# Kernel tuning notes

Measured on AMD Instinct MI355X. Metric: run time of the kernel, lower is better.

## Reference

```python
import jax, jax.numpy as jnp
import numpy as np
import math

B, T, D = 8, 2048, 1024
H, DH = 16, 64
DI = H * DH
EPS = 1e-6
LN_EPS = 1e-5


def setup_inputs() -> dict:
    key = jax.random.key(0)
    ks = jax.random.split(key, 8)
    def xavier(k, shape):
        fan_in, fan_out = shape[0], shape[1]
        bound = math.sqrt(6.0 / (fan_in + fan_out))
        return jax.random.uniform(k, shape, jnp.float32, -bound, bound)
    x = jax.random.normal(ks[0], (B, T, D), jnp.float32)
    Wq = xavier(ks[1], (D, DI))
    Wk = xavier(ks[2], (D, DI))
    Wv = xavier(ks[3], (D, DI))
    Wa = jax.random.normal(ks[4], (D, DI), jnp.float32) * 0.02
    ba = jnp.full((DI,), 3.0, jnp.float32)
    Wb = jax.random.normal(ks[5], (D, H), jnp.float32) * 0.02
    bb = jnp.zeros((H,), jnp.float32)
    raw_gamma_m = jnp.full((H,), math.log(0.99 / 0.01), jnp.float32)
    Wo = xavier(ks[6], (DI, D))
    ln_g = jnp.ones((D,), jnp.float32)
    ln_b = jnp.zeros((D,), jnp.float32)
    return {"x": x, "ln_g": ln_g, "ln_b": ln_b, "Wq": Wq, "Wk": Wk, "Wv": Wv,
            "Wa": Wa, "ba": ba, "Wb": Wb, "bb": bb,
            "raw_gamma_m": raw_gamma_m, "Wo": Wo}


def _layernorm(x, g, b):
    mu = jnp.mean(x, axis=-1, keepdims=True)
    var = jnp.mean(jnp.square(x - mu), axis=-1, keepdims=True)
    return (x - mu) * jax.lax.rsqrt(var + LN_EPS) * g + b


def _sokda_scan(q, k, v, alpha, beta, gamma_m):
    # q,k,v,alpha: (B,H,T,d); beta: (B,H,T); gamma_m: (H,)
    d = q.shape[-1]
    S0 = jnp.zeros((B, H, d, d), q.dtype)
    M0 = EPS * jnp.broadcast_to(jnp.eye(d, dtype=q.dtype), (B, H, d, d))
    gm = gamma_m[None, :, None, None]  # (1,H,1,1)

    def step(carry, xs):
        S, M = carry
        k_t, v_t, q_t, a_t, b_t = xs  # (B,H,d)x4, (B,H)
        kn = k_t / jnp.maximum(jnp.linalg.norm(k_t, axis=-1, keepdims=True), 1e-12)
        M = gm * M + kn[..., :, None] * kn[..., None, :]
        Mk = jnp.einsum('bhij,bhj->bhi', M, kn)
        k_tilde = Mk / jnp.maximum(jnp.linalg.norm(Mk, axis=-1, keepdims=True), EPS)
        S = a_t[..., None] * S  # diag(alpha) scaling of rows
        kproj = jnp.einsum('bhd,bhde->bhe', kn, S)  # k^T S
        bexp = b_t[..., None, None]
        S = S - bexp * k_tilde[..., :, None] * kproj[..., None, :]
        S = S + bexp * kn[..., :, None] * v_t[..., None, :]
        o = jnp.einsum('bhji,bhj->bhi', S, q_t)  # S^T q
        return (S, M), o

    # move time to leading axis for scan
    xs = (jnp.moveaxis(k, 2, 0), jnp.moveaxis(v, 2, 0), jnp.moveaxis(q, 2, 0),
          jnp.moveaxis(alpha, 2, 0), jnp.moveaxis(beta, 2, 0))
    _, outs = jax.lax.scan(step, (S0, M0), xs)  # outs: (T,B,H,d)
    return jnp.moveaxis(outs, 0, 2)  # (B,H,T,d)


def reference(x, ln_g, ln_b, Wq, Wk, Wv, Wa, ba, Wb, bb, raw_gamma_m, Wo):
    residual = x
    xn = _layernorm(x, ln_g, ln_b)
    def heads(y):
        return jnp.transpose(y.reshape(B, T, H, DH), (0, 2, 1, 3))  # (B,H,T,d)
    q = heads(xn @ Wq)
    k = heads(xn @ Wk)
    v = heads(xn @ Wv)
    alpha = jax.nn.sigmoid(heads(xn @ Wa + ba))
    beta = jnp.transpose(jax.nn.sigmoid(xn @ Wb + bb), (0, 2, 1))  # (B,H,T)
    gamma_m = jax.nn.sigmoid(raw_gamma_m)
    out = _sokda_scan(q, k, v, alpha, beta, gamma_m)  # (B,H,T,d)
    out = jnp.transpose(out, (0, 2, 1, 3)).reshape(B, T, DI)
    out = out @ Wo  # dropout is identity in eval mode
    return out + residual
```

## Files before the change

kernel.cpp:

```cpp
#include <hip/hip_runtime.h>

typedef unsigned short u16;
typedef unsigned int   u32;
typedef _Float16       f16;
typedef __attribute__((ext_vector_type(4))) _Float16 v4h;
typedef __attribute__((ext_vector_type(8))) _Float16 v8h;
typedef __attribute__((ext_vector_type(4))) float    v4f;

#define TT 2048
#define BB 8

static __device__ __forceinline__ float sigmoidf_(float x){
    return 1.0f / (1.0f + __expf(-x));
}
static __device__ __forceinline__ float allreduce64(float v){
    #pragma unroll
    for (int off = 32; off > 0; off >>= 1) v += __shfl_xor(v, off, 64);
    return v;
}

static __device__ __forceinline__ float wave_sum64(float x){
    int t;
    t = __builtin_amdgcn_update_dpp(0, __float_as_int(x), 0x111, 0xf, 0xf, true); x += __int_as_float(t);
    t = __builtin_amdgcn_update_dpp(0, __float_as_int(x), 0x112, 0xf, 0xf, true); x += __int_as_float(t);
    t = __builtin_amdgcn_update_dpp(0, __float_as_int(x), 0x114, 0xf, 0xf, true); x += __int_as_float(t);
    t = __builtin_amdgcn_update_dpp(0, __float_as_int(x), 0x118, 0xf, 0xf, true); x += __int_as_float(t);
    t = __builtin_amdgcn_update_dpp(0, __float_as_int(x), 0x142, 0xf, 0xf, true); x += __int_as_float(t);
    t = __builtin_amdgcn_update_dpp(0, __float_as_int(x), 0x143, 0xf, 0xf, true); x += __int_as_float(t);
    return __int_as_float(__builtin_amdgcn_readlane(__float_as_int(x), 63));
}
static __device__ __forceinline__ float rlane(float v, int lane){
    return __int_as_float(__builtin_amdgcn_readlane(__float_as_int(v), lane));
}

__global__ __launch_bounds__(256) void sentinel_fill(float* __restrict__ out, int n){
    int i = blockIdx.x * 256 + threadIdx.x;
    if (i < n) out[i] = 12345.0f;
}

__global__ __launch_bounds__(256) void ln_kernel(
    const float* __restrict__ x, const float* __restrict__ g,
    const float* __restrict__ bta, f16* __restrict__ xn)
{
    const int row = blockIdx.x;
    const int tid = threadIdx.x;
    const float4 v = ((const float4*)(x + (size_t)row * 1024))[tid];
    float s  = v.x + v.y + v.z + v.w;
    float s2 = v.x*v.x + v.y*v.y + v.z*v.z + v.w*v.w;
    #pragma unroll
    for (int off = 32; off > 0; off >>= 1){
        s  += __shfl_xor(s,  off, 64);
        s2 += __shfl_xor(s2, off, 64);
    }
    __shared__ float rs[4], rq[4];
    const int wv = tid >> 6, lane = tid & 63;
    if (lane == 0){ rs[wv] = s; rq[wv] = s2; }
    __syncthreads();
    s  = rs[0] + rs[1] + rs[2] + rs[3];
    s2 = rq[0] + rq[1] + rq[2] + rq[3];
    const float mu   = s * (1.0f / 1024.0f);
    const float var  = s2 * (1.0f / 1024.0f) - mu * mu;
    const float rstd = rsqrtf(var + 1e-5f);
    const float4 gv = ((const float4*)g)[tid];
    const float4 bv = ((const float4*)bta)[tid];
    v4h o;
    o.x = (f16)((v.x - mu) * rstd * gv.x + bv.x);
    o.y = (f16)((v.y - mu) * rstd * gv.y + bv.y);
    o.z = (f16)((v.z - mu) * rstd * gv.z + bv.z);
    o.w = (f16)((v.w - mu) * rstd * gv.w + bv.w);
    ((v4h*)(xn + (size_t)row * 1024))[tid] = o;
}

__global__ __launch_bounds__(256) void transpose5(
    const float* __restrict__ Wq, const float* __restrict__ Wk,
    const float* __restrict__ Wv, const float* __restrict__ Wa,
    const float* __restrict__ Wo, f16* __restrict__ wcat, f16* __restrict__ wot)
{
    __shared__ float tile[32][33];
    const int z = blockIdx.z;
    const float* src = (z==0)?Wq:(z==1)?Wk:(z==2)?Wv:(z==3)?Wa:Wo;
    f16* dst = (z < 4) ? (wcat + (size_t)z * 1024 * 1024) : wot;
    const int bx = blockIdx.x * 32, by = blockIdx.y * 32;
    const int tx = threadIdx.x, ty = threadIdx.y;
    #pragma unroll
    for (int i = 0; i < 4; ++i)
        tile[ty + i*8][tx] = src[(size_t)(by + ty + i*8) * 1024 + bx + tx];
    __syncthreads();
    #pragma unroll
    for (int i = 0; i < 4; ++i)
        dst[(size_t)(bx + ty + i*8) * 1024 + by + tx] = (f16)tile[tx][ty + i*8];
}

template<int MODE>
__global__ __launch_bounds__(256) void gemm_bt(
    const f16* __restrict__ A, const f16* __restrict__ Bt,
    int M, int N, int K,
    const float* __restrict__ ba, const float* __restrict__ resid,
    float* __restrict__ Cf,
    f16* __restrict__ Qb, f16* __restrict__ Kb,
    f16* __restrict__ Vb, f16* __restrict__ Ab)
{
    __shared__ f16 As[128 * 72];
    __shared__ f16 Bs[128 * 72];
    const int tid = threadIdx.x;
    const int bm = blockIdx.x, bn = blockIdx.y;
    const int wv = tid >> 6, lane = tid & 63;
    const int l15 = lane & 15, quad = lane >> 4;
    const int mb = (wv >> 1) * 64, nb = (wv & 1) * 64;
    v4f acc[4][4];
    const v4f vzero = {0.0f, 0.0f, 0.0f, 0.0f};
    #pragma unroll
    for (int i = 0; i < 4; ++i)
        #pragma unroll
        for (int j = 0; j < 4; ++j) acc[i][j] = vzero;

    const f16* Ag = A  + (size_t)bm * 128 * K;
    const f16* Bg = Bt + (size_t)bn * 128 * K;

    for (int k0 = 0; k0 < K; k0 += 64){
        __syncthreads();
        #pragma unroll
        for (int it = 0; it < 4; ++it){
            const int ch = tid + it * 256;
            const int r = ch >> 3, c = ch & 7;
            const uint4 da = *(const uint4*)(Ag + (size_t)r * K + k0 + c * 8);
            *(uint4*)(&As[r * 72 + c * 8]) = da;
            const uint4 db = *(const uint4*)(Bg + (size_t)r * K + k0 + c * 8);
            *(uint4*)(&Bs[r * 72 + c * 8]) = db;
        }
        __syncthreads();
        #pragma unroll
        for (int kk = 0; kk < 2; ++kk){
            v8h af[4], bfr[4];
            #pragma unroll
            for (int i = 0; i < 4; ++i){
                af[i]  = *(const v8h*)(&As[(mb + i*16 + l15) * 72 + kk*32 + quad*8]);
                bfr[i] = *(const v8h*)(&Bs[(nb + i*16 + l15) * 72 + kk*32 + quad*8]);
            }
            #pragma unroll
            for (int i = 0; i < 4; ++i)
                #pragma unroll
                for (int j = 0; j < 4; ++j)
                    acc[i][j] = __builtin_amdgcn_mfma_f32_16x16x32_f16(af[i], bfr[j], acc[i][j], 0, 0, 0);
        }
    }
    const int seg = (bn * 128) >> 10;
    f16* dst = (seg == 0) ? Qb : (seg == 1) ? Kb : (seg == 2) ? Vb : Ab;
    #pragma unroll
    for (int i = 0; i < 4; ++i){
        #pragma unroll
        for (int j = 0; j < 4; ++j){
            const int col = bn * 128 + nb + j * 16 + l15;
            const int c   = col & 1023;
            #pragma unroll
            for (int r = 0; r < 4; ++r){
                const int row = bm * 128 + mb + i * 16 + quad * 4 + r;
                float val = acc[i][j][r];
                if (MODE == 0){
                    if (seg == 3) val = sigmoidf_(val + ba[c]);
                    dst[(size_t)row * 1024 + c] = (f16)val;
                } else {
                    Cf[(size_t)row * N + col] = val + resid[(size_t)row * N + col];
                }
            }
        }
    }
}

__global__ __launch_bounds__(256) void beta_kernel(
    const f16* __restrict__ xn, const float* __restrict__ Wb,
    const float* __restrict__ bb, float* __restrict__ betaw)
{
    const int row = blockIdx.x;
    const int b = row >> 11, t = row & 2047;
    const int wv = threadIdx.x >> 6, lane = threadIdx.x & 63;
    const f16* xr = xn + (size_t)row * 1024;
    #pragma unroll
    for (int hh = 0; hh < 4; ++hh){
        const int h = wv * 4 + hh;
        float acc = 0.0f;
        #pragma unroll 4
        for (int k = lane; k < 1024; k += 64)
            acc += (float)xr[k] * Wb[k * 16 + h];
        acc = allreduce64(acc);
        if (lane == 0)
            betaw[((size_t)(b * 16 + h)) * 2048 + t] = sigmoidf_(acc + bb[h]);
    }
}

#define SC 16
__global__ __launch_bounds__(512, 2) void scan_kernel(
    const f16* __restrict__ Qb, const f16* __restrict__ Kb,
    const f16* __restrict__ Vb, const f16* __restrict__ Ab,
    const float* __restrict__ beta, const float* __restrict__ rgm,
    f16* __restrict__ O)
{
    const int chain = blockIdx.x;
    const int b = chain >> 4, h = chain & 15;
    const int tid = threadIdx.x;
    const int wid = __builtin_amdgcn_readfirstlane(tid) >> 6;
    const int l = tid & 63;
    const int jbase = wid << 3;
    const float gm = sigmoidf_(rgm[h]);
    const int l15 = l & 15, q4 = l >> 4;

    __shared__ f16 tQ[1024], tK[1024], tV[1024], tA[1024];
    __shared__ float betaT[SC], rnkT[SC];
    __shared__ float ktlT[1024];
    __shared__ float Gc[1024];
    __shared__ float mkP[8192];
    __shared__ f16 PhT[16*72], PlT[16*72], QhT[16*72], QlT[16*72];
    __shared__ f16 Wcat[16*136], Ucat[16*136];
    __shared__ f16 WTcat[64*40], UTcat[64*40];
    __shared__ f16 HTcat[64*40];
    __shared__ f16 VT[64*24];
    __shared__ f16 ZTcat[64*136];
    __shared__ f16 Cmcat[3*16*40];
    __shared__ float ZsT[64*68];
    __shared__ float Hs[16*68], Ob[16*68];
    __shared__ float C2s[16*17];

    float m[8];
    #pragma unroll
    for (int dd = 0; dd < 8; ++dd)
        m[dd] = (jbase + dd == l) ? 1e-6f : 0.0f;

    const size_t cbase = ((size_t)(b * TT)) * 1024 + h * 64;
    const int tens = tid >> 7, rem = tid & 127;
    const int str = rem >> 3, j4 = rem & 7;
    const f16* sg = (tens == 0) ? Qb : (tens == 1) ? Kb : (tens == 2) ? Vb : Ab;
    f16* sl = (tens == 0) ? tQ : (tens == 1) ? tK : (tens == 2) ? tV : tA;

    {
        const uint4 d0 = *(const uint4*)(sg + cbase + (size_t)str * 1024 + j4 * 8);
        *(uint4*)(sl + str * 64 + j4 * 8) = d0;
        if (tid < SC) betaT[tid] = beta[(size_t)chain * TT + tid];
        for (int i = tid; i < 64*68; i += 512) ZsT[i] = 0.0f;
        for (int i = tid; i < 64*136; i += 512) ZTcat[i] = (f16)0.0f;
    }

    #pragma unroll 1
    for (int t0 = 0; t0 < TT; t0 += SC){
        __syncthreads();

        #pragma unroll
        for (int rr = 0; rr < 2; ++rr){
            const int t = (wid << 1) + rr;
            const float kv = (float)tK[t * 64 + l];
            const float nk = wave_sum64(kv * kv);
            if (l == 0) rnkT[t] = __builtin_amdgcn_rcpf(fmaxf(sqrtf(nk), 1e-12f));
        }
        if (wid == 7){
            float g = 1.0f;
            #pragma unroll
            for (int t = 0; t < SC; ++t){
                g *= (float)tA[t * 64 + l];
                Gc[t * 64 + l] = g;
            }
        }
        __syncthreads();

        #pragma unroll
        for (int t = 0; t < SC; ++t){
            const float knl = (float)tK[t * 64 + l] * rnkT[t];
            float knj2[8];
            #pragma unroll
            for (int dd = 0; dd < 8; ++dd) knj2[dd] = rlane(knl, jbase + dd);
            float mk0 = 0.f, mk1 = 0.f;
            #pragma unroll
            for (int dd = 0; dd < 8; dd += 2){
                m[dd]     = fmaf(gm, m[dd],     knl * knj2[dd]);
                mk0 = fmaf(m[dd], knj2[dd], mk0);
                m[dd + 1] = fmaf(gm, m[dd + 1], knl * knj2[dd + 1]);
                mk1 = fmaf(m[dd + 1], knj2[dd + 1], mk1);
            }
            mkP[(t << 9) + (wid << 6) + l] = mk0 + mk1;
        }
        __syncthreads();

        #pragma unroll
        for (int rr = 0; rr < 2; ++rr){
            const int t = (wid << 1) + rr;
            float mkf = 0.f;
            #pragma unroll
            for (int w2 = 0; w2 < 8; ++w2) mkf += mkP[(t << 9) + (w2 << 6) + l];
            const float nmk = wave_sum64(mkf * mkf);
            ktlT[t * 64 + l] = mkf * __builtin_amdgcn_rcpf(fmaxf(sqrtf(nmk), 1e-6f));
        }
        #pragma unroll
        for (int half = 0; half < 2; ++half){
            const int idx = tid + half * 512;
            const int e = idx & 63, i = idx >> 6;
            VT[e * 24 + i] = tV[i * 64 + e];
        }
        __syncthreads();

        #pragma unroll
        for (int half = 0; half < 2; ++half){
            const int idx = tid + half * 512;
            const int t = idx >> 6, d = idx & 63;
            const float g    = Gc[t * 64 + d];
            const float invg = 1.0f / g;
            const float kn   = (float)tK[t * 64 + d] * rnkT[t];
            const float bt   = betaT[t];
            const float pv = kn * g;
            const float uv = bt * ktlT[t * 64 + d] * invg;
            const float wv = bt * kn * invg;
            const float qv = (float)tQ[t * 64 + d] * g;
            const f16 ph = (f16)pv, qh = (f16)qv, wh = (f16)wv, uh = (f16)uv;
            const f16 pl = (f16)(pv - (float)ph), ql = (f16)(qv - (float)qh);
            const f16 wl = (f16)(wv - (float)wh), ul = (f16)(uv - (float)uh);
            PhT[t * 72 + d] = ph;  PlT[t * 72 + d] = pl;
            QhT[t * 72 + d] = qh;  QlT[t * 72 + d] = ql;
            const int cc = ((d >> 4) << 5) + (d & 15);
            Wcat[t * 136 + cc] = wh;  Wcat[t * 136 + cc + 16] = wl;
            Ucat[t * 136 + cc] = uh;  Ucat[t * 136 + cc + 16] = ul;
            WTcat[d * 40 + t] = wh;   WTcat[d * 40 + 16 + t] = wl;
            const float nuv = -uv;
            const f16 nuh = (f16)nuv;
            UTcat[d * 40 + t] = nuh;  UTcat[d * 40 + 16 + t] = (f16)(nuv - (float)nuh);
        }
        __syncthreads();

        {
            const int et = wid & 3;
            const f16* Amh = (wid < 4) ? PhT : QhT;
            const f16* Aml = (wid < 4) ? PlT : QlT;
            const int ar = l15 * 72 + (q4 & 1) * 8;
            const int br = (et * 16 + l15) * 136 + q4 * 8;
            v4f acc = {0.f, 0.f, 0.f, 0.f};
            #pragma unroll
            for (int c = 0; c < 4; ++c){
                const v8h ah = *(const v8h*)(Amh + ar + c * 16);
                const v8h al = *(const v8h*)(Aml + ar + c * 16);
                const v8h bz = *(const v8h*)(ZTcat + br + c * 32);
                acc = __builtin_amdgcn_mfma_f32_16x16x32_f16(ah, bz, acc, 0, 0, 0);
                acc = __builtin_amdgcn_mfma_f32_16x16x32_f16(al, bz, acc, 0, 0, 0);
            }
            float* Rdst = (wid < 4) ? Hs : Ob;
            #pragma unroll
            for (int j = 0; j < 4; ++j)
                Rdst[(q4 * 4 + j) * 68 + et * 16 + l15] = acc[j];

            if (wid < 4){
                const f16* A2h = (wid < 2) ? PhT : QhT;
                const f16* A2l = (wid < 2) ? PlT : QlT;
                const f16* Bp  = (wid & 1) ? Ucat : Wcat;
                const int br2 = l15 * 136 + q4 * 8;
                v4f pacc = {0.f, 0.f, 0.f, 0.f};
                #pragma unroll
                for (int c = 0; c < 4; ++c){
                    const v8h a2h = *(const v8h*)(A2h + ar + c * 16);
                    const v8h a2l = *(const v8h*)(A2l + ar + c * 16);
                    const v8h bw  = *(const v8h*)(Bp + br2 + c * 32);
                    pacc = __builtin_amdgcn_mfma_f32_16x16x32_f16(a2h, bw, pacc, 0, 0, 0);
                    pacc = __builtin_amdgcn_mfma_f32_16x16x32_f16(a2l, bw, pacc, 0, 0, 0);
                }
                if (wid == 1){
                    #pragma unroll
                    for (int j = 0; j < 4; ++j)
                        C2s[(q4 * 4 + j) * 17 + l15] = pacc[j];
                } else {
                    const int mm = (wid == 0) ? 0 : (wid == 2) ? 1 : 2;
                    #pragma unroll
                    for (int j = 0; j < 4; ++j){
                        const int t = q4 * 4 + j, i = l15;
                        float v = ((mm == 0) ? (i < t) : (i <= t)) ? pacc[j] : 0.0f;
                        if (mm == 2) v = -v;
                        const f16 vh = (f16)v;
                        Cmcat[mm * 640 + t * 40 + i] = vh;
                        Cmcat[mm * 640 + t * 40 + 16 + i] = (f16)(v - (float)vh);
                    }
                }
            }
        }
        __syncthreads();

        {
            const int et = wid & 3;
            const int mm = (wid < 4) ? 0 : 1;
            float* Rd = (wid < 4) ? Hs : Ob;
            const v8h ac = *(const v8h*)(Cmcat + mm * 640 + l15 * 40 + q4 * 8);
            const v8h bv = *(const v8h*)(VT + (et * 16 + l15) * 24 + (q4 & 1) * 8);
            v4f acc;
            #pragma unroll
            for (int j = 0; j < 4; ++j) acc[j] = Rd[(q4 * 4 + j) * 68 + et * 16 + l15];
            acc = __builtin_amdgcn_mfma_f32_16x16x32_f16(ac, bv, acc, 0, 0, 0);
            #pragma unroll
            for (int j = 0; j < 4; ++j) Rd[(q4 * 4 + j) * 68 + et * 16 + l15] = acc[j];
        }
        __syncthreads();

        if (wid == 0){
            float hreg[SC];
            #pragma unroll
            for (int t = 0; t < SC; ++t){
                float x = Hs[t * 68 + l];
                #pragma unroll
                for (int i = 0; i < SC; ++i)
                    if (i < t) x = fmaf(-C2s[t * 17 + i], hreg[i], x);
                hreg[t] = x;
                const f16 hh = (f16)x;
                HTcat[l * 40 + t] = hh;
                HTcat[l * 40 + 16 + t] = (f16)(x - (float)hh);
            }
        } else if (t0 + SC < TT){
            const int base = tid - 64;
            #pragma unroll
            for (int rep = 0; rep < 2; ++rep){
                const int ch = base + rep * 448;
                if (ch < 512){
                    const int tens2 = ch >> 7, rem2 = ch & 127;
                    const int str2 = rem2 >> 3, jj = rem2 & 7;
                    const f16* sgp = (tens2 == 0) ? Qb : (tens2 == 1) ? Kb : (tens2 == 2) ? Vb : Ab;
                    f16* slp = (tens2 == 0) ? tQ : (tens2 == 1) ? tK : (tens2 == 2) ? tV : tA;
                    const uint4 dd0 = *(const uint4*)(sgp + cbase + (size_t)(t0 + SC + str2) * 1024 + jj * 8);
                    *(uint4*)(slp + str2 * 64 + jj * 8) = dd0;
                }
            }
            if (base < SC) betaT[base] = beta[(size_t)chain * TT + t0 + SC + base];
        }
        __syncthreads();

        {
            const int et = wid & 3;
            const int arow = et * 16 + l15;
            const v8h aV  = *(const v8h*)(VT + arow * 24 + (q4 & 1) * 8);
            const v8h aHh = *(const v8h*)(HTcat + arow * 40 + (q4 & 1) * 8);
            const v8h aHl = *(const v8h*)(HTcat + arow * 40 + 16 + (q4 & 1) * 8);

            if (wid < 4){
                const v8h aC = *(const v8h*)(Cmcat + 2 * 640 + l15 * 40 + q4 * 8);
                v4f acc2;
                #pragma unroll
                for (int j = 0; j < 4; ++j) acc2[j] = Ob[(q4 * 4 + j) * 68 + et * 16 + l15];
                acc2 = __builtin_amdgcn_mfma_f32_16x16x32_f16(aC, aHh, acc2, 0, 0, 0);
                acc2 = __builtin_amdgcn_mfma_f32_16x16x32_f16(aC, aHl, acc2, 0, 0, 0);
                #pragma unroll
                for (int j = 0; j < 4; ++j){
                    const int t = q4 * 4 + j;
                    O[cbase + (size_t)(t0 + t) * 1024 + et * 16 + l15] = (f16)acc2[j];
                }
            }

            #pragma unroll
            for (int tt2 = 0; tt2 < 2; ++tt2){
                const int dt = (wid >> 2) * 2 + tt2;
                const v8h bW = *(const v8h*)(WTcat + (dt * 16 + l15) * 40 + q4 * 8);
                const v8h bU = *(const v8h*)(UTcat + (dt * 16 + l15) * 40 + q4 * 8);
                v4f acc;
                #pragma unroll
                for (int j = 0; j < 4; ++j)
                    acc[j] = ZsT[(et * 16 + q4 * 4 + j) * 68 + dt * 16 + l15];
                acc = __builtin_amdgcn_mfma_f32_16x16x32_f16(aV,  bW, acc, 0, 0, 0);
                acc = __builtin_amdgcn_mfma_f32_16x16x32_f16(aHh, bU, acc, 0, 0, 0);
                acc = __builtin_amdgcn_mfma_f32_16x16x32_f16(aHl, bU, acc, 0, 0, 0);
                const float gl = Gc[15 * 64 + dt * 16 + l15];
                #pragma unroll
                for (int j = 0; j < 4; ++j){
                    const float z = acc[j] * gl;
                    const int er = et * 16 + q4 * 4 + j;
                    ZsT[er * 68 + dt * 16 + l15] = z;
                    const f16 zh = (f16)z;
                    ZTcat[er * 136 + dt * 32 + l15] = zh;
                    ZTcat[er * 136 + dt * 32 + 16 + l15] = (f16)(z - (float)zh);
                }
            }
        }
    }
}

#define OFF_XN    ((size_t)0)
#define OFF_WCAT  ((size_t)33554432)
#define OFF_WOT   ((size_t)41943040)
#define OFF_BETA  ((size_t)44040192)
#define OFF_V     ((size_t)45088768)
#define OFF_A     ((size_t)78643200)
#define WS_NEED   ((size_t)112197632)

extern "C" void kernel_launch(void* const* d_in, const int* in_sizes, int n_in,
                              void* d_out, int out_size, void* d_ws, size_t ws_size,
                              hipStream_t stream)
{
    const float* x   = (const float*)d_in[0];
    const float* lng = (const float*)d_in[1];
    const float* lnb = (const float*)d_in[2];
    const float* Wq  = (const float*)d_in[3];
    const float* Wk  = (const float*)d_in[4];
    const float* Wv  = (const float*)d_in[5];
    const float* Wa  = (const float*)d_in[6];
    const float* ba  = (const float*)d_in[7];
    const float* Wb  = (const float*)d_in[8];
    const float* bb  = (const float*)d_in[9];
    const float* rgm = (const float*)d_in[10];
    const float* Wo  = (const float*)d_in[11];
    float* out = (float*)d_out;

    if (ws_size < WS_NEED){
        sentinel_fill<<<(out_size + 255) / 256, 256, 0, stream>>>(out, out_size);
        return;
    }

    char* ws = (char*)d_ws;
    f16*   xn   = (f16*)(ws + OFF_XN);
    f16*   wcat = (f16*)(ws + OFF_WCAT);
    f16*   wot  = (f16*)(ws + OFF_WOT);
    float* betw = (float*)(ws + OFF_BETA);
    f16*   Vbuf = (f16*)(ws + OFF_V);
    f16*   Abuf = (f16*)(ws + OFF_A);
    f16*   Qbuf = (f16*)d_out;
    f16*   Kbuf = Qbuf + (size_t)16384 * 1024;
    f16*   Obuf = xn;

    ln_kernel<<<16384, 256, 0, stream>>>(x, lng, lnb, xn);
    transpose5<<<dim3(32, 32, 5), dim3(32, 8), 0, stream>>>(Wq, Wk, Wv, Wa, Wo, wcat, wot);
    gemm_bt<0><<<dim3(128, 32), 256, 0, stream>>>(xn, wcat, 16384, 4096, 1024,
                                                  ba, nullptr, nullptr, Qbuf, Kbuf, Vbuf, Abuf);
    beta_kernel<<<16384, 256, 0, stream>>>(xn, Wb, bb, betw);
    scan_kernel<<<128, 512, 0, stream>>>(Qbuf, Kbuf, Vbuf, Abuf, betw, rgm, Obuf);
    gemm_bt<1><<<dim3(128, 8), 256, 0, stream>>>(Obuf, wot, 16384, 1024, 1024,
                                                 nullptr, x, out, nullptr, nullptr, nullptr, nullptr);
}
```

Measured before the change: 1.725 ms.

## Compute M-matrix recurrence chunkwise with MFMA instead of per-step register updates

Replaces the per-timestep serial update of the key second-moment matrix M (register FMAs plus lane broadcasts and a partial-sum reduction through shared memory) with a chunked formulation. Within each 16-step chunk it builds a decayed Gram matrix of normalized keys and uses MFMA products against the carried M0 to get all Mk vectors at once, then updates M0 with one rank-16 MFMA at the end of the chunk. The M0 update runs on waves that previously only prefetched. It also drops the fp32 Z state copy, reconstructing it from the hi/lo f16 split, which saves shared memory. Storing M and Z as split f16 pairs and the extra barriers could cost accuracy and add sync overhead.

Result: no change. 1.711 ms (-0.8%).

```diff
diff --git a/kernel.cpp b/kernel.cpp
--- a/kernel.cpp
+++ b/kernel.cpp
@@ -28,9 +28,6 @@
     t = __builtin_amdgcn_update_dpp(0, __float_as_int(x), 0x142, 0xf, 0xf, true); x += __int_as_float(t);
     t = __builtin_amdgcn_update_dpp(0, __float_as_int(x), 0x143, 0xf, 0xf, true); x += __int_as_float(t);
     return __int_as_float(__builtin_amdgcn_readlane(__float_as_int(x), 63));
-}
-static __device__ __forceinline__ float rlane(float v, int lane){
-    return __int_as_float(__builtin_amdgcn_readlane(__float_as_int(v), lane));
 }
 
 __global__ __launch_bounds__(256) void sentinel_fill(float* __restrict__ out, int n){
@@ -200,15 +197,17 @@
     const int tid = threadIdx.x;
     const int wid = __builtin_amdgcn_readfirstlane(tid) >> 6;
     const int l = tid & 63;
-    const int jbase = wid << 3;
     const float gm = sigmoidf_(rgm[h]);
     const int l15 = l & 15, q4 = l >> 4;
 
     __shared__ f16 tQ[1024], tK[1024], tV[1024], tA[1024];
-    __shared__ float betaT[SC], rnkT[SC];
-    __shared__ float ktlT[1024];
-    __shared__ float Gc[1024];
-    __shared__ float mkP[8192];
+    __shared__ float betaT[SC], rnkT[SC], gmps[20];
+    __shared__ float GcT[64*18], IGcT[64*18], ktlTT[64*18];
+    __shared__ f16 KnAh[16*72], KnAl[16*72];
+    __shared__ f16 KnBcat[16*136];
+    __shared__ f16 KnTcat[64*40], KnTEcat[64*40];
+    __shared__ f16 Dcat[16*40];
+    __shared__ f16 M0h[64*72], M0l[64*72];
     __shared__ f16 PhT[16*72], PlT[16*72], QhT[16*72], QlT[16*72];
     __shared__ f16 Wcat[16*136], Ucat[16*136];
     __shared__ f16 WTcat[64*40], UTcat[64*40];
@@ -216,14 +215,8 @@
     __shared__ f16 VT[64*24];
     __shared__ f16 ZTcat[64*136];
     __shared__ f16 Cmcat[3*16*40];
-    __shared__ float ZsT[64*68];
     __shared__ float Hs[16*68], Ob[16*68];
     __shared__ float C2s[16*17];
-
-    float m[8];
-    #pragma unroll
-    for (int dd = 0; dd < 8; ++dd)
-        m[dd] = (jbase + dd == l) ? 1e-6f : 0.0f;
 
     const size_t cbase = ((size_t)(b * TT)) * 1024 + h * 64;
     const int tens = tid >> 7, rem = tid & 127;
@@ -235,9 +228,16 @@
         const uint4 d0 = *(const uint4*)(sg + cbase + (size_t)str * 1024 + j4 * 8);
         *(uint4*)(sl + str * 64 + j4 * 8) = d0;
         if (tid < SC) betaT[tid] = beta[(size_t)chain * TT + tid];
-        for (int i = tid; i < 64*68; i += 512) ZsT[i] = 0.0f;
         for (int i = tid; i < 64*136; i += 512) ZTcat[i] = (f16)0.0f;
+        for (int i = tid; i < 64*72; i += 512){ M0h[i] = (f16)0.0f; M0l[i] = (f16)0.0f; }
+        if (tid == 0){
+            float g = 1.0f;
+            #pragma unroll
+            for (int k = 0; k <= 16; ++k){ gmps[k] = g; g *= gm; }
+        }
     }
+    __syncthreads();
+    if (tid < 64) M0h[tid * 73] = (f16)1e-6f;
 
     #pragma unroll 1
     for (int t0 = 0; t0 < TT; t0 += SC){
@@ -255,70 +255,155 @@
             #pragma unroll
             for (int t = 0; t < SC; ++t){
                 g *= (float)tA[t * 64 + l];
-                Gc[t * 64 + l] = g;
+                GcT[l * 18 + t]  = g;
+                IGcT[l * 18 + t] = __builtin_amdgcn_rcpf(g);
             }
         }
         __syncthreads();
 
         #pragma unroll
-        for (int t = 0; t < SC; ++t){
-            const float knl = (float)tK[t * 64 + l] * rnkT[t];
-            float knj2[8];
-            #pragma unroll
-            for (int dd = 0; dd < 8; ++dd) knj2[dd] = rlane(knl, jbase + dd);
-            float mk0 = 0.f, mk1 = 0.f;
-            #pragma unroll
-            for (int dd = 0; dd < 8; dd += 2){
-                m[dd]     = fmaf(gm, m[dd],     knl * knj2[dd]);
-                mk0 = fmaf(m[dd], knj2[dd], mk0);
-                m[dd + 1] = fmaf(gm, m[dd + 1], knl * knj2[dd + 1]);
-                mk1 = fmaf(m[dd + 1], knj2[dd + 1], mk1);
-            }
-            mkP[(t << 9) + (wid << 6) + l] = mk0 + mk1;
+        for (int half = 0; half < 2; ++half){
+            const int idx = tid + half * 512;
+            {
+                const int t = idx >> 6, d = idx & 63;
+                const float kn = (float)tK[t * 64 + d] * rnkT[t];
+                const f16 kh = (f16)kn; const f16 kl = (f16)(kn - (float)kh);
+                KnAh[t * 72 + d] = kh;  KnAl[t * 72 + d] = kl;
+                const int cc = ((d >> 4) << 5) + (d & 15);
+                KnBcat[t * 136 + cc] = kh;  KnBcat[t * 136 + cc + 16] = kl;
+            }
+            {
+                const int d2 = idx >> 4, t2 = idx & 15;
+                const float kn2 = (float)tK[t2 * 64 + d2] * rnkT[t2];
+                const f16 kh2 = (f16)kn2;
+                KnTcat[d2 * 40 + t2]      = kh2;
+                KnTcat[d2 * 40 + 16 + t2] = (f16)(kn2 - (float)kh2);
+                const float ke = kn2 * gmps[15 - t2];
+                const f16 keh = (f16)ke;
+                KnTEcat[d2 * 40 + t2]      = keh;
+                KnTEcat[d2 * 40 + 16 + t2] = (f16)(ke - (float)keh);
+            }
+            {
+                const int e = idx & 63, i2 = idx >> 6;
+                VT[e * 24 + i2] = tV[i2 * 64 + e];
+            }
+        }
+        __syncthreads();
+
+        if (wid == 0){
+            const int ar = l15 * 72 + (q4 & 1) * 8;
+            const int br = l15 * 136 + q4 * 8;
+            v4f g4 = {0.f, 0.f, 0.f, 0.f};
+            #pragma unroll
+            for (int c = 0; c < 4; ++c)
+                g4 = __builtin_amdgcn_mfma_f32_16x16x32_f16(
+                        *(const v8h*)(KnAh + ar + c * 16),
+                        *(const v8h*)(KnBcat + br + c * 32), g4, 0, 0, 0);
+            #pragma unroll
+            for (int c = 0; c < 4; ++c)
+                g4 = __builtin_amdgcn_mfma_f32_16x16x32_f16(
+                        *(const v8h*)(KnAl + ar + c * 16),
+                        *(const v8h*)(KnBcat + br + c * 32), g4, 0, 0, 0);
+            #pragma unroll
+            for (int j = 0; j < 4; ++j){
+                const int t = q4 * 4 + j, i = l15;
+                const float dv = (i <= t) ? g4[j] * gmps[t - i] : 0.0f;
+                const f16 dh = (f16)dv;
+                Dcat[t * 40 + i]      = dh;
+                Dcat[t * 40 + 16 + i] = (f16)(dv - (float)dh);
+            }
+        } else if (wid <= 4){
+            const int rt = wid - 1;
+            const int ar = (rt * 16 + l15) * 72 + (q4 & 1) * 8;
+            const int br = l15 * 136 + q4 * 8;
+            v4f acc = {0.f, 0.f, 0.f, 0.f};
+            #pragma unroll
+            for (int c = 0; c < 4; ++c)
+                acc = __builtin_amdgcn_mfma_f32_16x16x32_f16(
+                        *(const v8h*)(M0h + ar + c * 16),
+                        *(const v8h*)(KnBcat + br + c * 32), acc, 0, 0, 0);
+            #pragma unroll
+            for (int c = 0; c < 4; ++c)
+                acc = __builtin_amdgcn_mfma_f32_16x16x32_f16(
+                        *(const v8h*)(M0l + ar + c * 16),
+                        *(const v8h*)(KnBcat + br + c * 32), acc, 0, 0, 0);
+            #pragma unroll
+            for (int j = 0; j < 4; ++j)
+                Hs[(rt * 16 + q4 * 4 + j) * 17 + l15] = acc[j];
+        }
+        __syncthreads();
+
+        if (wid < 4){
+            const int et = wid;
+            const int arD = l15 * 40 + (q4 & 1) * 8;
+            const int brD = (et * 16 + l15) * 40 + q4 * 8;
+            v4f acc = {0.f, 0.f, 0.f, 0.f};
+            acc = __builtin_amdgcn_mfma_f32_16x16x32_f16(
+                    *(const v8h*)(Dcat + arD), *(const v8h*)(KnTcat + brD), acc, 0, 0, 0);
+            acc = __builtin_amdgcn_mfma_f32_16x16x32_f16(
+                    *(const v8h*)(Dcat + arD + 16), *(const v8h*)(KnTcat + brD), acc, 0, 0, 0);
+            #pragma unroll
+            for (int j = 0; j < 4; ++j){
+                const int t = q4 * 4 + j, d = et * 16 + l15;
+                Ob[t * 68 + d] = acc[j] + gmps[t + 1] * Hs[d * 17 + t];
+            }
+        } else {
+            #pragma unroll
+            for (int k = 0; k < 4; ++k){
+                const int idx = (tid - 256) + k * 256;
+                const int t = idx >> 6, d = idx & 63;
+                const float g  = GcT[d * 18 + t];
+                const float ig = IGcT[d * 18 + t];
+                const float kn = (float)tK[t * 64 + d] * rnkT[t];
+                const float bt = betaT[t];
+                const float pv = kn * g;
+                const float qv = (float)tQ[t * 64 + d] * g;
+                const float wv = bt * kn * ig;
+                const f16 ph = (f16)pv, qh = (f16)qv, wh = (f16)wv;
+                PhT[t * 72 + d] = ph;  PlT[t * 72 + d] = (f16)(pv - (float)ph);
+                QhT[t * 72 + d] = qh;  QlT[t * 72 + d] = (f16)(qv - (float)qh);
+                const int cc = ((d >> 4) << 5) + (d & 15);
+                Wcat[t * 136 + cc] = wh;  Wcat[t * 136 + cc + 16] = (f16)(wv - (float)wh);
+            }
         }
         __syncthreads();
 
         #pragma unroll
         for (int rr = 0; rr < 2; ++rr){
             const int t = (wid << 1) + rr;
-            float mkf = 0.f;
-            #pragma unroll
-            for (int w2 = 0; w2 < 8; ++w2) mkf += mkP[(t << 9) + (w2 << 6) + l];
-            const float nmk = wave_sum64(mkf * mkf);
-            ktlT[t * 64 + l] = mkf * __builtin_amdgcn_rcpf(fmaxf(sqrtf(nmk), 1e-6f));
-        }
-        #pragma unroll
-        for (int half = 0; half < 2; ++half){
-            const int idx = tid + half * 512;
-            const int e = idx & 63, i = idx >> 6;
-            VT[e * 24 + i] = tV[i * 64 + e];
-        }
-        __syncthreads();
-
-        #pragma unroll
-        for (int half = 0; half < 2; ++half){
-            const int idx = tid + half * 512;
-            const int t = idx >> 6, d = idx & 63;
-            const float g    = Gc[t * 64 + d];
-            const float invg = 1.0f / g;
-            const float kn   = (float)tK[t * 64 + d] * rnkT[t];
-            const float bt   = betaT[t];
-            const float pv = kn * g;
-            const float uv = bt * ktlT[t * 64 + d] * invg;
-            const float wv = bt * kn * invg;
-            const float qv = (float)tQ[t * 64 + d] * g;
-            const f16 ph = (f16)pv, qh = (f16)qv, wh = (f16)wv, uh = (f16)uv;
-            const f16 pl = (f16)(pv - (float)ph), ql = (f16)(qv - (float)qh);
-            const f16 wl = (f16)(wv - (float)wh), ul = (f16)(uv - (float)uh);
-            PhT[t * 72 + d] = ph;  PlT[t * 72 + d] = pl;
-            QhT[t * 72 + d] = qh;  QlT[t * 72 + d] = ql;
-            const int cc = ((d >> 4) << 5) + (d & 15);
-            Wcat[t * 136 + cc] = wh;  Wcat[t * 136 + cc + 16] = wl;
-            Ucat[t * 136 + cc] = uh;  Ucat[t * 136 + cc + 16] = ul;
-            WTcat[d * 40 + t] = wh;   WTcat[d * 40 + 16 + t] = wl;
-            const float nuv = -uv;
-            const f16 nuh = (f16)nuv;
-            UTcat[d * 40 + t] = nuh;  UTcat[d * 40 + 16 + t] = (f16)(nuv - (float)nuh);
+            const float x = Ob[t * 68 + l];
+            const float nm = wave_sum64(x * x);
+            ktlTT[l * 18 + t] = x * __builtin_amdgcn_rcpf(fmaxf(sqrtf(nm), 1e-6f));
+        }
+        __syncthreads();
+
+        if (wid < 4){
+            #pragma unroll
+            for (int k = 0; k < 4; ++k){
+                const int idx = tid + k * 256;
+                const int t = idx >> 6, d = idx & 63;
+                const float uv = betaT[t] * ktlTT[d * 18 + t] * IGcT[d * 18 + t];
+                const f16 uh = (f16)uv;
+                const int cc = ((d >> 4) << 5) + (d & 15);
+                Ucat[t * 136 + cc] = uh;  Ucat[t * 136 + cc + 16] = (f16)(uv - (float)uh);
+            }
+        } else {
+            #pragma unroll
+            for (int k = 0; k < 4; ++k){
+                const int idx = (tid - 256) + k * 256;
+                const int d = idx >> 4, t = idx & 15;
+                const float ig = IGcT[d * 18 + t];
+                const float bt = betaT[t];
+                const float kn = (float)KnTcat[d * 40 + t] + (float)KnTcat[d * 40 + 16 + t];
+                const float wv = bt * kn * ig;
+                const f16 wh = (f16)wv;
+                WTcat[d * 40 + t]      = wh;
+                WTcat[d * 40 + 16 + t] = (f16)(wv - (float)wh);
+                const float nu = -(bt * ktlTT[d * 18 + t] * ig);
+                const f16 nuh = (f16)nu;
+                UTcat[d * 40 + t]      = nuh;
+                UTcat[d * 40 + 16 + t] = (f16)(nu - (float)nuh);
+            }
         }
         __syncthreads();
 
@@ -392,10 +477,13 @@
         __syncthreads();
 
         if (wid == 0){
+            float rhs[SC];
+            #pragma unroll
+            for (int t = 0; t < SC; ++t) rhs[t] = Hs[t * 68 + l];
             float hreg[SC];
             #pragma unroll
             for (int t = 0; t < SC; ++t){
-                float x = Hs[t * 68 + l];
+                float x = rhs[t];
                 #pragma unroll
                 for (int i = 0; i < SC; ++i)
                     if (i < t) x = fmaf(-C2s[t * 17 + i], hreg[i], x);
@@ -404,21 +492,51 @@
                 HTcat[l * 40 + t] = hh;
                 HTcat[l * 40 + 16 + t] = (f16)(x - (float)hh);
             }
-        } else if (t0 + SC < TT){
-            const int base = tid - 64;
-            #pragma unroll
-            for (int rep = 0; rep < 2; ++rep){
-                const int ch = base + rep * 448;
-                if (ch < 512){
-                    const int tens2 = ch >> 7, rem2 = ch & 127;
-                    const int str2 = rem2 >> 3, jj = rem2 & 7;
-                    const f16* sgp = (tens2 == 0) ? Qb : (tens2 == 1) ? Kb : (tens2 == 2) ? Vb : Ab;
-                    f16* slp = (tens2 == 0) ? tQ : (tens2 == 1) ? tK : (tens2 == 2) ? tV : tA;
-                    const uint4 dd0 = *(const uint4*)(sgp + cbase + (size_t)(t0 + SC + str2) * 1024 + jj * 8);
-                    *(uint4*)(slp + str2 * 64 + jj * 8) = dd0;
-                }
-            }
-            if (base < SC) betaT[base] = beta[(size_t)chain * TT + t0 + SC + base];
+        } else {
+            if (t0 + SC < TT){
+                const int base = tid - 64;
+                #pragma unroll
+                for (int rep = 0; rep < 2; ++rep){
+                    const int ch = base + rep * 448;
+                    if (ch < 512){
+                        const int tens2 = ch >> 7, rem2 = ch & 127;
+                        const int str2 = rem2 >> 3, jj = rem2 & 7;
+                        const f16* sgp = (tens2 == 0) ? Qb : (tens2 == 1) ? Kb : (tens2 == 2) ? Vb : Ab;
+                        f16* slp = (tens2 == 0) ? tQ : (tens2 == 1) ? tK : (tens2 == 2) ? tV : tA;
+                        const uint4 dd0 = *(const uint4*)(sgp + cbase + (size_t)(t0 + SC + str2) * 1024 + jj * 8);
+                        *(uint4*)(slp + str2 * 64 + jj * 8) = dd0;
+                    }
+                }
+                if (base < SC) betaT[base] = beta[(size_t)chain * TT + t0 + SC + base];
+            }
+            const float gm16 = gmps[16];
+            #pragma unroll
+            for (int r = 0; r < 3; ++r){
+                const int tile = (wid - 1) + 7 * r;
+                if (tile < 16){
+                    const int rt = tile >> 2, ct = tile & 3;
+                    const int ar = (rt * 16 + l15) * 40 + (q4 & 1) * 8;
+                    const int br = (ct * 16 + l15) * 40 + q4 * 8;
+                    v4f acc;
+                    #pragma unroll
+                    for (int j = 0; j < 4; ++j){
+                        const int row = rt * 16 + q4 * 4 + j, col = ct * 16 + l15;
+                        acc[j] = gm16 * ((float)M0h[row * 72 + col] + (float)M0l[row * 72 + col]);
+                    }
+                    acc = __builtin_amdgcn_mfma_f32_16x16x32_f16(
+                            *(const v8h*)(KnTcat + ar), *(const v8h*)(KnTEcat + br), acc, 0, 0, 0);
+                    acc = __builtin_amdgcn_mfma_f32_16x16x32_f16(
+                            *(const v8h*)(KnTcat + ar + 16), *(const v8h*)(KnTEcat + br), acc, 0, 0, 0);
+                    #pragma unroll
+                    for (int j = 0; j < 4; ++j){
+                        const int row = rt * 16 + q4 * 4 + j, col = ct * 16 + l15;
+                        const float v = acc[j];
+                        const f16 vh = (f16)v;
+                        M0h[row * 72 + col] = vh;
+                        M0l[row * 72 + col] = (f16)(v - (float)vh);
+                    }
+                }
+            }
         }
         __syncthreads();
 
@@ -450,17 +568,19 @@
                 const v8h bU = *(const v8h*)(UTcat + (dt * 16 + l15) * 40 + q4 * 8);
                 v4f acc;
                 #pragma unroll
-                for (int j = 0; j < 4; ++j)
-                    acc[j] = ZsT[(et * 16 + q4 * 4 + j) * 68 + dt * 16 + l15];
+                for (int j = 0; j < 4; ++j){
+                    const int er = et * 16 + q4 * 4 + j;
+                    acc[j] = (float)ZTcat[er * 136 + dt * 32 + l15]
+                           + (float)ZTcat[er * 136 + dt * 32 + 16 + l15];
+                }
                 acc = __builtin_amdgcn_mfma_f32_16x16x32_f16(aV,  bW, acc, 0, 0, 0);
                 acc = __builtin_amdgcn_mfma_f32_16x16x32_f16(aHh, bU, acc, 0, 0, 0);
                 acc = __builtin_amdgcn_mfma_f32_16x16x32_f16(aHl, bU, acc, 0, 0, 0);
-                const float gl = Gc[15 * 64 + dt * 16 + l15];
+                const float gl = GcT[(dt * 16 + l15) * 18 + 15];
                 #pragma unroll
                 for (int j = 0; j < 4; ++j){
                     const float z = acc[j] * gl;
                     const int er = et * 16 + q4 * 4 + j;
-                    ZsT[er * 68 + dt * 16 + l15] = z;
                     const f16 zh = (f16)z;
                     ZTcat[er * 136 + dt * 32 + l15] = zh;
                     ZTcat[er * 136 + dt * 32 + 16 + l15] = (f16)(z - (float)zh);
```
